# Optimization experiments

Hardware: AMD Instinct MI355X
Metric: run time of the kernel (lower is better)

The kernel has to match this reference:

```python
import jax, jax.numpy as jnp
import numpy as np


def setup_inputs() -> dict:
    key = jax.random.key(0)
    k1, k2 = jax.random.split(key)
    B, Q, K, H = 8, 2048, 2048, 128
    out_state = jax.random.normal(k1, (B, Q, H), dtype=jnp.float32)
    history = jax.random.normal(k2, (B, K, H), dtype=jnp.float32)
    return {"out_state": out_state, "history": history}


def reference(out_state, history):
    # tanh pre-activation on queries
    q = jnp.tanh(out_state)                              # [B, Q, H]
    # unscaled QK^T scores
    scores = jnp.einsum("bqh,bkh->bqk", q, history)      # [B, Q, K]
    probs = jax.nn.softmax(scores, axis=2)               # softmax over keys
    attn = jnp.einsum("bqk,bkh->bqh", probs, history)    # [B, Q, H]
    return attn
```

## Files before the change

kernel.cpp:

```cpp
#include <hip/hip_runtime.h>
#include <math.h>


typedef _Float16 half8 __attribute__((ext_vector_type(8)));
typedef _Float16 half4 __attribute__((ext_vector_type(4)));
typedef float    f32x4 __attribute__((ext_vector_type(4)));

#define QQ 2048
#define KK 2048
#define HH 128
#define BM 64
#define BN 64
#define NTILES 32
#define PS_STR 72
#define L2E 1.44269504f
#define SPLITS_TARGET 3

#define KS_STRP 136
#define VT_STRP 72

#define KH_HALVES     ((size_t)8 * KK * HH)
#define PREP_BYTES    (KH_HALVES * 4)
#define OSPLIT_BYTES  ((size_t)256 * BM * HH * 2)
#define MLSPLIT_FLOATS ((size_t)256 * BM)

union U32H { unsigned int u; _Float16 h[2]; };

typedef __attribute__((address_space(1))) const void gvoid;
typedef __attribute__((address_space(3))) void lvoid;

#define WAITVM4 asm volatile("s_waitcnt vmcnt(4)" ::: "memory")
#define WAITVM0 asm volatile("s_waitcnt vmcnt(0)" ::: "memory")
static __device__ __forceinline__ void wgbar() {
    asm volatile("" ::: "memory");
    __builtin_amdgcn_s_barrier();
    asm volatile("" ::: "memory");
}

__launch_bounds__(256)
__global__ void attn_prep(const float* __restrict__ history,
                          _Float16* __restrict__ wsh) {
    __shared__ __align__(16) _Float16 Ks[BN * KS_STRP];
    __shared__ __align__(16) _Float16 Vt[HH * VT_STRP];

    const int tid = threadIdx.x;
    const int bid = blockIdx.x;
    const int b   = bid >> 5;
    const int kt  = bid & 31;

    const float* hb = history + ((size_t)b * KK + (size_t)kt * BN) * HH;
    const int r0 = tid >> 5;
    const int c4 = (tid & 31) * 4;
    #pragma unroll
    for (int j = 0; j < 8; ++j) {
        const float4 g = *(const float4*)(hb + (size_t)(r0 + 8 * j) * HH + c4);
        half4 hv;
        hv[0] = (_Float16)g.x; hv[1] = (_Float16)g.y;
        hv[2] = (_Float16)g.z; hv[3] = (_Float16)g.w;
        *(half4*)&Ks[(r0 + 8 * j) * KS_STRP + c4] = hv;
    }
    __syncthreads();

    {
        const int h0  = 2 * (tid & 63);
        const int n0t = (tid >> 6) * 16;
        half8 ra0, ra1, rb0, rb1;
        #pragma unroll
        for (int i = 0; i < 8; ++i) {
            U32H t; t.u = *(const unsigned int*)&Ks[(n0t + i) * KS_STRP + h0];
            ra0[i] = t.h[0]; rb0[i] = t.h[1];
        }
        #pragma unroll
        for (int i = 8; i < 16; ++i) {
            U32H t; t.u = *(const unsigned int*)&Ks[(n0t + i) * KS_STRP + h0];
            ra1[i - 8] = t.h[0]; rb1[i - 8] = t.h[1];
        }
        *(half8*)&Vt[(h0    ) * VT_STRP + n0t    ] = ra0;
        *(half8*)&Vt[(h0    ) * VT_STRP + n0t + 8] = ra1;
        *(half8*)&Vt[(h0 + 1) * VT_STRP + n0t    ] = rb0;
        *(half8*)&Vt[(h0 + 1) * VT_STRP + n0t + 8] = rb1;
    }

    {
        const int k  = tid >> 2;
        const int c0 = (tid & 3) * 32;
        const int sk = (k & 7) << 3;
        _Float16* dst = wsh + ((size_t)b * KK + (size_t)kt * BN + k) * HH;
        #pragma unroll
        for (int g8 = 0; g8 < 4; ++g8)
            *(half8*)&dst[(c0 + 8 * g8) ^ sk] = *(const half8*)&Ks[k * KS_STRP + c0 + 8 * g8];
    }
    __syncthreads();

    {
        const int h  = tid >> 1;
        const int n0 = (tid & 1) * 32;
        const int th = (h & 7) << 3;
        _Float16* dst = wsh + KH_HALVES + (((size_t)b * NTILES + kt) * HH + h) * BN;
        #pragma unroll
        for (int g8 = 0; g8 < 4; ++g8)
            *(half8*)&dst[(n0 + 8 * g8) ^ th] = *(const half8*)&Vt[h * VT_STRP + n0 + 8 * g8];
    }
}

__launch_bounds__(256, 3)
__global__ void attn_main(const float* __restrict__ out_state,
                          const _Float16* __restrict__ wsh,
                          float* __restrict__ out,
                          char* __restrict__ wsb,
                          int splits) {
    __shared__ __align__(16) _Float16 Ks[BN * HH];
    __shared__ __align__(16) _Float16 Vt[HH * BN];
    __shared__ __align__(16) _Float16 Ps[4][16 * PS_STR];

    const int tid  = threadIdx.x;
    const int wave = tid >> 6;
    const int lane = tid & 63;
    const int quad = lane >> 4;
    const int lc   = lane & 15;
    const int swz  = (lc & 7) << 3;

    const int bid  = blockIdx.x;
    const int s    = bid >> 8;
    const int r256 = bid & 255;
    const int b    = r256 >> 5;
    const int qb   = r256 & 31;
    const int m0   = qb * BM;

    const int kt0 = (NTILES * s) / splits;
    const int kt1 = (NTILES * (s + 1)) / splits;

    const _Float16* khb = wsh + (size_t)b * KK * HH;
    const _Float16* vtb = wsh + KH_HALVES + (size_t)b * NTILES * (HH * BN);

    auto issueK = [&](int t) {
        const char* gsrc = (const char*)(khb + (size_t)t * (BN * HH));
        #pragma unroll
        for (int c = 0; c < 4; ++c) {
            const int off = (c * 4 + wave) * 1024 + lane * 16;
            __builtin_amdgcn_global_load_lds((gvoid*)(gsrc + off),
                                             (lvoid*)((char*)Ks + off), 16, 0, 0);
        }
    };
    auto issueV = [&](int t) {
        const char* gsrc = (const char*)(vtb + (size_t)t * (HH * BN));
        #pragma unroll
        for (int c = 0; c < 4; ++c) {
            const int off = (c * 4 + wave) * 1024 + lane * 16;
            __builtin_amdgcn_global_load_lds((gvoid*)(gsrc + off),
                                             (lvoid*)((char*)Vt + off), 16, 0, 0);
        }
    };

    issueK(kt0);
    issueV(kt0);

    half8 qf[4];
    {
        const int m = m0 + wave * 16 + lc;
        const float* qrow = out_state + ((size_t)b * QQ + m) * HH;
        float4 qa[8];
        #pragma unroll
        for (int s4 = 0; s4 < 4; ++s4) {
            qa[2 * s4]     = *(const float4*)(qrow + 32 * s4 + quad * 8);
            qa[2 * s4 + 1] = *(const float4*)(qrow + 32 * s4 + quad * 8 + 4);
        }
        #pragma unroll
        for (int s4 = 0; s4 < 4; ++s4) {
            qf[s4][0] = (_Float16)tanhf(qa[2*s4].x);   qf[s4][1] = (_Float16)tanhf(qa[2*s4].y);
            qf[s4][2] = (_Float16)tanhf(qa[2*s4].z);   qf[s4][3] = (_Float16)tanhf(qa[2*s4].w);
            qf[s4][4] = (_Float16)tanhf(qa[2*s4+1].x); qf[s4][5] = (_Float16)tanhf(qa[2*s4+1].y);
            qf[s4][6] = (_Float16)tanhf(qa[2*s4+1].z); qf[s4][7] = (_Float16)tanhf(qa[2*s4+1].w);
        }
    }

    const f32x4 zero4 = {0.f, 0.f, 0.f, 0.f};
    f32x4 O[8];
    #pragma unroll
    for (int i = 0; i < 8; ++i) O[i] = zero4;
    f32x4 Osum = zero4;
    float rmax = -3.0e38f;

    const half8 ones = {(_Float16)1.f,(_Float16)1.f,(_Float16)1.f,(_Float16)1.f,
                        (_Float16)1.f,(_Float16)1.f,(_Float16)1.f,(_Float16)1.f};

    for (int kt = kt0; kt < kt1; ++kt) {
        const bool more = (kt + 1 < kt1);

        WAITVM4;
        wgbar();

        f32x4 S[4];
        __builtin_amdgcn_s_setprio(1);
        #pragma unroll
        for (int nt = 0; nt < 4; ++nt) {
            f32x4 acc = zero4;
            #pragma unroll
            for (int s4 = 0; s4 < 4; ++s4) {
                const half8 kf = *(const half8*)
                    &Ks[((nt * 16 + lc) << 7) + ((32 * s4 + (quad << 3)) ^ swz)];
                acc = __builtin_amdgcn_mfma_f32_16x16x32_f16(kf, qf[s4], acc, 0, 0, 0);
            }
            S[nt] = acc;
        }
        __builtin_amdgcn_s_setprio(0);

        wgbar();
        if (more) issueK(kt + 1);

        float tmax = S[0][0];
        #pragma unroll
        for (int nt = 0; nt < 4; ++nt)
            #pragma unroll
            for (int r = 0; r < 4; ++r)
                tmax = fmaxf(tmax, S[nt][r]);
        tmax = fmaxf(tmax, __shfl_xor(tmax, 16, 64));
        tmax = fmaxf(tmax, __shfl_xor(tmax, 32, 64));

        if (!__all(tmax <= rmax)) {
            const float nm    = fmaxf(rmax, tmax);
            const float alpha = exp2f((rmax - nm) * L2E);
            rmax = nm;
            #pragma unroll
            for (int ct = 0; ct < 8; ++ct) O[ct] *= alpha;
            Osum *= alpha;
        }

        #pragma unroll
        for (int nt = 0; nt < 4; ++nt)
            #pragma unroll
            for (int r = 0; r < 4; ++r)
                S[nt][r] = exp2f((S[nt][r] - rmax) * L2E);

        #pragma unroll
        for (int nt = 0; nt < 4; ++nt) {
            half4 pv;
            pv[0] = (_Float16)S[nt][0]; pv[1] = (_Float16)S[nt][1];
            pv[2] = (_Float16)S[nt][2]; pv[3] = (_Float16)S[nt][3];
            *(half4*)&Ps[wave][lc * PS_STR + nt * 16 + quad * 4] = pv;
        }

        if (more) { WAITVM4; } else { WAITVM0; }
        wgbar();

        __builtin_amdgcn_s_setprio(1);
        #pragma unroll
        for (int s2 = 0; s2 < 2; ++s2) {
            const half8 pb = *(const half8*)&Ps[wave][lc * PS_STR + s2 * 32 + quad * 8];
            Osum = __builtin_amdgcn_mfma_f32_16x16x32_f16(ones, pb, Osum, 0, 0, 0);
            #pragma unroll
            for (int ct = 0; ct < 8; ++ct) {
                const half8 vf = *(const half8*)
                    &Vt[((ct * 16 + lc) << 6) + ((32 * s2 + (quad << 3)) ^ swz)];
                O[ct] = __builtin_amdgcn_mfma_f32_16x16x32_f16(vf, pb, O[ct], 0, 0, 0);
            }
        }
        __builtin_amdgcn_s_setprio(0);

        wgbar();
        if (more) issueV(kt + 1);
    }

    if (splits == 1) {
        const float inv = 1.0f / Osum[0];
        float* orow = out + ((size_t)b * QQ + m0 + wave * 16 + lc) * HH;
        #pragma unroll
        for (int ct = 0; ct < 8; ++ct) {
            f32x4 v = O[ct] * inv;
            *(f32x4*)&orow[ct * 16 + quad * 4] = v;
        }
    } else {
        const float inv = 1.0f / Osum[0];
        _Float16* oh = (_Float16*)(wsb + PREP_BYTES)
                     + ((size_t)(s * 256 + r256) * BM + wave * 16 + lc) * HH;
        #pragma unroll
        for (int ct = 0; ct < 8; ++ct) {
            const f32x4 v = O[ct] * inv;
            half4 hv;
            hv[0] = (_Float16)v[0]; hv[1] = (_Float16)v[1];
            hv[2] = (_Float16)v[2]; hv[3] = (_Float16)v[3];
            *(half4*)&oh[ct * 16 + quad * 4] = hv;
        }
        if (quad == 0) {
            float* wm = (float*)(wsb + PREP_BYTES + (size_t)splits * OSPLIT_BYTES);
            const size_t idx = (size_t)(s * 256 + r256) * BM + wave * 16 + lc;
            wm[idx] = rmax;
            wm[(size_t)splits * MLSPLIT_FLOATS + idx] = Osum[0];
        }
    }
}

__launch_bounds__(256)
__global__ void attn_combine(const char* __restrict__ wsb,
                             float* __restrict__ out,
                             int splits) {
    const int idx = blockIdx.x * 256 + threadIdx.x;
    const int h   = idx & 127;
    const int q   = (idx >> 7) & 2047;
    const int b   = idx >> 18;
    const int qb  = q >> 6;
    const int qr  = q & 63;
    const int blk = b * 32 + qb;

    const _Float16* oh = (const _Float16*)(wsb + PREP_BYTES);
    const float* wm = (const float*)(wsb + PREP_BYTES + (size_t)splits * OSPLIT_BYTES);
    const float* wl = wm + (size_t)splits * MLSPLIT_FLOATS;

    float ms[SPLITS_TARGET];
    float M = -3.0e38f;
    for (int s = 0; s < splits; ++s) {
        ms[s] = wm[(size_t)(s * 256 + blk) * BM + qr];
        M = fmaxf(M, ms[s]);
    }
    float denom = 0.f, val = 0.f;
    for (int s = 0; s < splits; ++s) {
        const float wgt = exp2f((ms[s] - M) * L2E) * wl[(size_t)(s * 256 + blk) * BM + qr];
        denom += wgt;
        val   += wgt * (float)oh[(size_t)(s * 256 + blk) * (BM * HH) + (size_t)qr * HH + h];
    }
    out[idx] = val / denom;
}

extern "C" void kernel_launch(void* const* d_in, const int* in_sizes, int n_in,
                              void* d_out, int out_size, void* d_ws, size_t ws_size,
                              hipStream_t stream) {
    const float* out_state = (const float*)d_in[0];
    const float* history   = (const float*)d_in[1];
    float* out = (float*)d_out;
    char* wsb  = (char*)d_ws;

    const size_t need3 = PREP_BYTES
                       + (size_t)SPLITS_TARGET * OSPLIT_BYTES
                       + (size_t)SPLITS_TARGET * 2 * MLSPLIT_FLOATS * 4;
    const int splits = (ws_size >= need3) ? SPLITS_TARGET : 1;

    attn_prep<<<dim3(256), dim3(256), 0, stream>>>(history, (_Float16*)wsb);
    attn_main<<<dim3(256 * splits), dim3(256), 0, stream>>>(out_state, (const _Float16*)wsb,
                                                            out, wsb, splits);
    if (splits > 1)
        attn_combine<<<dim3((8 * QQ * HH) / 256), dim3(256), 0, stream>>>(wsb, out, splits);
}
```

Measured before the change: 120.9 us.

## Fuse prep, main and combine into one cooperative kernel with grid syncs

Merges the three kernels (fp16 conversion/transpose of history, split attention, split combine) into one cooperative launch of 768 blocks that uses grid-wide syncs, removing two kernel launch gaps. The prep stage now writes swizzled tiles into LDS and copies them out linearly, and the combine handles two outputs per thread with vector stores. The cooperative path needs all 768 blocks resident at once (3 per CU on 256 CUs). It also adds the cost of grid barriers and falls back to separate launches if the cooperative launch fails.

```diff
diff --git a/kernel.cpp b/kernel.cpp
--- a/kernel.cpp
+++ b/kernel.cpp
@@ -1,10 +1,14 @@
 #include <hip/hip_runtime.h>
+#include <hip/hip_cooperative_groups.h>
 #include <math.h>
 
+
+namespace cg = cooperative_groups;
 
 typedef _Float16 half8 __attribute__((ext_vector_type(8)));
 typedef _Float16 half4 __attribute__((ext_vector_type(4)));
 typedef float    f32x4 __attribute__((ext_vector_type(4)));
+typedef float    f32x2 __attribute__((ext_vector_type(2)));
 
 #define QQ 2048
 #define KK 2048
@@ -14,15 +18,19 @@
 #define NTILES 32
 #define PS_STR 72
 #define L2E 1.44269504f
-#define SPLITS_TARGET 3
-
-#define KS_STRP 136
-#define VT_STRP 72
-
-#define KH_HALVES     ((size_t)8 * KK * HH)
-#define PREP_BYTES    (KH_HALVES * 4)
-#define OSPLIT_BYTES  ((size_t)256 * BM * HH * 2)
+#define SPLITS 3
+#define FUSED_BLOCKS (256 * SPLITS)
+
+#define KH_HALVES      ((size_t)8 * KK * HH)
+#define PREP_BYTES     (KH_HALVES * 4)
+#define OSPLIT_BYTES   ((size_t)256 * BM * HH * 2)
 #define MLSPLIT_FLOATS ((size_t)256 * BM)
+
+struct SharedMem {
+    _Float16 Ks[BN * HH];
+    _Float16 Vt[HH * BN];
+    _Float16 Ps[4][16 * PS_STR];
+};
 
 union U32H { unsigned int u; _Float16 h[2]; };
 
@@ -37,27 +45,23 @@
     asm volatile("" ::: "memory");
 }
 
-__launch_bounds__(256)
-__global__ void attn_prep(const float* __restrict__ history,
-                          _Float16* __restrict__ wsh) {
-    __shared__ __align__(16) _Float16 Ks[BN * KS_STRP];
-    __shared__ __align__(16) _Float16 Vt[HH * VT_STRP];
-
-    const int tid = threadIdx.x;
-    const int bid = blockIdx.x;
-    const int b   = bid >> 5;
-    const int kt  = bid & 31;
+static __device__ __forceinline__
+void do_prep(SharedMem* sm, const float* __restrict__ history,
+             _Float16* __restrict__ wsh, int bid, int tid) {
+    const int b  = bid >> 5;
+    const int kt = bid & 31;
 
     const float* hb = history + ((size_t)b * KK + (size_t)kt * BN) * HH;
     const int r0 = tid >> 5;
     const int c4 = (tid & 31) * 4;
     #pragma unroll
     for (int j = 0; j < 8; ++j) {
-        const float4 g = *(const float4*)(hb + (size_t)(r0 + 8 * j) * HH + c4);
+        const int k = r0 + 8 * j;
+        const float4 g = *(const float4*)(hb + (size_t)k * HH + c4);
         half4 hv;
         hv[0] = (_Float16)g.x; hv[1] = (_Float16)g.y;
         hv[2] = (_Float16)g.z; hv[3] = (_Float16)g.w;
-        *(half4*)&Ks[(r0 + 8 * j) * KS_STRP + c4] = hv;
+        *(half4*)&sm->Ks[k * HH + (c4 ^ ((k & 7) << 3))] = hv;
     }
     __syncthreads();
 
@@ -67,60 +71,46 @@
         half8 ra0, ra1, rb0, rb1;
         #pragma unroll
         for (int i = 0; i < 8; ++i) {
-            U32H t; t.u = *(const unsigned int*)&Ks[(n0t + i) * KS_STRP + h0];
+            const int n = n0t + i;
+            U32H t; t.u = *(const unsigned int*)&sm->Ks[n * HH + (h0 ^ ((n & 7) << 3))];
             ra0[i] = t.h[0]; rb0[i] = t.h[1];
         }
         #pragma unroll
         for (int i = 8; i < 16; ++i) {
-            U32H t; t.u = *(const unsigned int*)&Ks[(n0t + i) * KS_STRP + h0];
+            const int n = n0t + i;
+            U32H t; t.u = *(const unsigned int*)&sm->Ks[n * HH + (h0 ^ ((n & 7) << 3))];
             ra1[i - 8] = t.h[0]; rb1[i - 8] = t.h[1];
         }
-        *(half8*)&Vt[(h0    ) * VT_STRP + n0t    ] = ra0;
-        *(half8*)&Vt[(h0    ) * VT_STRP + n0t + 8] = ra1;
-        *(half8*)&Vt[(h0 + 1) * VT_STRP + n0t    ] = rb0;
-        *(half8*)&Vt[(h0 + 1) * VT_STRP + n0t + 8] = rb1;
-    }
-
-    {
-        const int k  = tid >> 2;
-        const int c0 = (tid & 3) * 32;
-        const int sk = (k & 7) << 3;
-        _Float16* dst = wsh + ((size_t)b * KK + (size_t)kt * BN + k) * HH;
-        #pragma unroll
-        for (int g8 = 0; g8 < 4; ++g8)
-            *(half8*)&dst[(c0 + 8 * g8) ^ sk] = *(const half8*)&Ks[k * KS_STRP + c0 + 8 * g8];
+        const int th0 = (h0 & 7) << 3;
+        const int th1 = ((h0 + 1) & 7) << 3;
+        *(half8*)&sm->Vt[(h0    ) * BN + ((n0t    ) ^ th0)] = ra0;
+        *(half8*)&sm->Vt[(h0    ) * BN + ((n0t + 8) ^ th0)] = ra1;
+        *(half8*)&sm->Vt[(h0 + 1) * BN + ((n0t    ) ^ th1)] = rb0;
+        *(half8*)&sm->Vt[(h0 + 1) * BN + ((n0t + 8) ^ th1)] = rb1;
     }
     __syncthreads();
 
-    {
-        const int h  = tid >> 1;
-        const int n0 = (tid & 1) * 32;
-        const int th = (h & 7) << 3;
-        _Float16* dst = wsh + KH_HALVES + (((size_t)b * NTILES + kt) * HH + h) * BN;
-        #pragma unroll
-        for (int g8 = 0; g8 < 4; ++g8)
-            *(half8*)&dst[(n0 + 8 * g8) ^ th] = *(const half8*)&Vt[h * VT_STRP + n0 + 8 * g8];
-    }
-}
-
-__launch_bounds__(256, 3)
-__global__ void attn_main(const float* __restrict__ out_state,
-                          const _Float16* __restrict__ wsh,
-                          float* __restrict__ out,
-                          char* __restrict__ wsb,
-                          int splits) {
-    __shared__ __align__(16) _Float16 Ks[BN * HH];
-    __shared__ __align__(16) _Float16 Vt[HH * BN];
-    __shared__ __align__(16) _Float16 Ps[4][16 * PS_STR];
-
-    const int tid  = threadIdx.x;
+    _Float16* kdst = wsh + ((size_t)b * KK + (size_t)kt * BN) * HH;
+    _Float16* vdst = wsh + KH_HALVES + ((size_t)(b * NTILES + kt)) * (HH * BN);
+    const f32x4* ksrc = (const f32x4*)sm->Ks;
+    const f32x4* vsrc = (const f32x4*)sm->Vt;
+    #pragma unroll
+    for (int i = 0; i < 4; ++i) {
+        ((f32x4*)kdst)[i * 256 + tid] = ksrc[i * 256 + tid];
+        ((f32x4*)vdst)[i * 256 + tid] = vsrc[i * 256 + tid];
+    }
+}
+
+static __device__ __forceinline__
+void do_main(SharedMem* sm, const float* __restrict__ out_state,
+             const _Float16* __restrict__ wsh, float* __restrict__ out,
+             char* __restrict__ wsb, int bid, int tid, int splits) {
     const int wave = tid >> 6;
     const int lane = tid & 63;
     const int quad = lane >> 4;
     const int lc   = lane & 15;
     const int swz  = (lc & 7) << 3;
 
-    const int bid  = blockIdx.x;
     const int s    = bid >> 8;
     const int r256 = bid & 255;
     const int b    = r256 >> 5;
@@ -139,7 +129,7 @@
         for (int c = 0; c < 4; ++c) {
             const int off = (c * 4 + wave) * 1024 + lane * 16;
             __builtin_amdgcn_global_load_lds((gvoid*)(gsrc + off),
-                                             (lvoid*)((char*)Ks + off), 16, 0, 0);
+                                             (lvoid*)((char*)sm->Ks + off), 16, 0, 0);
         }
     };
     auto issueV = [&](int t) {
@@ -148,7 +138,7 @@
         for (int c = 0; c < 4; ++c) {
             const int off = (c * 4 + wave) * 1024 + lane * 16;
             __builtin_amdgcn_global_load_lds((gvoid*)(gsrc + off),
-                                             (lvoid*)((char*)Vt + off), 16, 0, 0);
+                                             (lvoid*)((char*)sm->Vt + off), 16, 0, 0);
         }
     };
 
@@ -198,7 +188,7 @@
             #pragma unroll
             for (int s4 = 0; s4 < 4; ++s4) {
                 const half8 kf = *(const half8*)
-                    &Ks[((nt * 16 + lc) << 7) + ((32 * s4 + (quad << 3)) ^ swz)];
+                    &sm->Ks[((nt * 16 + lc) << 7) + ((32 * s4 + (quad << 3)) ^ swz)];
                 acc = __builtin_amdgcn_mfma_f32_16x16x32_f16(kf, qf[s4], acc, 0, 0, 0);
             }
             S[nt] = acc;
@@ -237,7 +227,7 @@
             half4 pv;
             pv[0] = (_Float16)S[nt][0]; pv[1] = (_Float16)S[nt][1];
             pv[2] = (_Float16)S[nt][2]; pv[3] = (_Float16)S[nt][3];
-            *(half4*)&Ps[wave][lc * PS_STR + nt * 16 + quad * 4] = pv;
+            *(half4*)&sm->Ps[wave][lc * PS_STR + nt * 16 + quad * 4] = pv;
         }
 
         if (more) { WAITVM4; } else { WAITVM0; }
@@ -246,12 +236,12 @@
         __builtin_amdgcn_s_setprio(1);
         #pragma unroll
         for (int s2 = 0; s2 < 2; ++s2) {
-            const half8 pb = *(const half8*)&Ps[wave][lc * PS_STR + s2 * 32 + quad * 8];
+            const half8 pb = *(const half8*)&sm->Ps[wave][lc * PS_STR + s2 * 32 + quad * 8];
             Osum = __builtin_amdgcn_mfma_f32_16x16x32_f16(ones, pb, Osum, 0, 0, 0);
             #pragma unroll
             for (int ct = 0; ct < 8; ++ct) {
                 const half8 vf = *(const half8*)
-                    &Vt[((ct * 16 + lc) << 6) + ((32 * s2 + (quad << 3)) ^ swz)];
+                    &sm->Vt[((ct * 16 + lc) << 6) + ((32 * s2 + (quad << 3)) ^ swz)];
                 O[ct] = __builtin_amdgcn_mfma_f32_16x16x32_f16(vf, pb, O[ct], 0, 0, 0);
             }
         }
@@ -290,14 +280,12 @@
     }
 }
 
-__launch_bounds__(256)
-__global__ void attn_combine(const char* __restrict__ wsb,
-                             float* __restrict__ out,
-                             int splits) {
-    const int idx = blockIdx.x * 256 + threadIdx.x;
-    const int h   = idx & 127;
-    const int q   = (idx >> 7) & 2047;
-    const int b   = idx >> 18;
+static __device__ __forceinline__
+void do_combine_pair(const char* __restrict__ wsb, float* __restrict__ out,
+                     int pid, int splits) {
+    const int h2  = pid & 63;
+    const int q   = (pid >> 6) & 2047;
+    const int b   = pid >> 17;
     const int qb  = q >> 6;
     const int qr  = q & 63;
     const int blk = b * 32 + qb;
@@ -306,19 +294,69 @@
     const float* wm = (const float*)(wsb + PREP_BYTES + (size_t)splits * OSPLIT_BYTES);
     const float* wl = wm + (size_t)splits * MLSPLIT_FLOATS;
 
-    float ms[SPLITS_TARGET];
+    float ms[SPLITS];
     float M = -3.0e38f;
     for (int s = 0; s < splits; ++s) {
         ms[s] = wm[(size_t)(s * 256 + blk) * BM + qr];
         M = fmaxf(M, ms[s]);
     }
-    float denom = 0.f, val = 0.f;
+    float denom = 0.f, v0 = 0.f, v1 = 0.f;
     for (int s = 0; s < splits; ++s) {
         const float wgt = exp2f((ms[s] - M) * L2E) * wl[(size_t)(s * 256 + blk) * BM + qr];
         denom += wgt;
-        val   += wgt * (float)oh[(size_t)(s * 256 + blk) * (BM * HH) + (size_t)qr * HH + h];
-    }
-    out[idx] = val / denom;
+        U32H t;
+        t.u = *(const unsigned int*)&oh[(size_t)(s * 256 + blk) * (BM * HH)
+                                        + (size_t)qr * HH + 2 * h2];
+        v0 += wgt * (float)t.h[0];
+        v1 += wgt * (float)t.h[1];
+    }
+    const float inv = 1.0f / denom;
+    f32x2 r; r[0] = v0 * inv; r[1] = v1 * inv;
+    *(f32x2*)&out[((size_t)(b * QQ + q)) * HH + 2 * h2] = r;
+}
+
+__launch_bounds__(256, 3)
+__global__ void attn_fused(const float* __restrict__ out_state,
+                           const float* __restrict__ history,
+                           float* __restrict__ out,
+                           char* __restrict__ wsb) {
+    __shared__ SharedMem sm;
+    const int tid = threadIdx.x;
+    const int bid = blockIdx.x;
+
+    if (bid < 256)
+        do_prep(&sm, history, (_Float16*)wsb, bid, tid);
+    cg::this_grid().sync();
+
+    do_main(&sm, out_state, (const _Float16*)wsb, out, wsb, bid, tid, SPLITS);
+    cg::this_grid().sync();
+
+    for (int pid = bid * 256 + tid; pid < (1 << 20); pid += FUSED_BLOCKS * 256)
+        do_combine_pair(wsb, out, pid, SPLITS);
+}
+
+__launch_bounds__(256)
+__global__ void attn_prep_k(const float* __restrict__ history,
+                            _Float16* __restrict__ wsh) {
+    __shared__ SharedMem sm;
+    do_prep(&sm, history, wsh, blockIdx.x, threadIdx.x);
+}
+
+__launch_bounds__(256, 3)
+__global__ void attn_main_k(const float* __restrict__ out_state,
+                            const _Float16* __restrict__ wsh,
+                            float* __restrict__ out,
+                            char* __restrict__ wsb,
+                            int splits) {
+    __shared__ SharedMem sm;
+    do_main(&sm, out_state, wsh, out, wsb, blockIdx.x, threadIdx.x, splits);
+}
+
+__launch_bounds__(256)
+__global__ void attn_combine_k(const char* __restrict__ wsb,
+                               float* __restrict__ out,
+                               int splits) {
+    do_combine_pair(wsb, out, blockIdx.x * 256 + threadIdx.x, splits);
 }
 
 extern "C" void kernel_launch(void* const* d_in, const int* in_sizes, int n_in,
@@ -330,13 +368,23 @@
     char* wsb  = (char*)d_ws;
 
     const size_t need3 = PREP_BYTES
-                       + (size_t)SPLITS_TARGET * OSPLIT_BYTES
-                       + (size_t)SPLITS_TARGET * 2 * MLSPLIT_FLOATS * 4;
-    const int splits = (ws_size >= need3) ? SPLITS_TARGET : 1;
-
-    attn_prep<<<dim3(256), dim3(256), 0, stream>>>(history, (_Float16*)wsb);
-    attn_main<<<dim3(256 * splits), dim3(256), 0, stream>>>(out_state, (const _Float16*)wsb,
-                                                            out, wsb, splits);
-    if (splits > 1)
-        attn_combine<<<dim3((8 * QQ * HH) / 256), dim3(256), 0, stream>>>(wsb, out, splits);
-}
+                       + (size_t)SPLITS * OSPLIT_BYTES
+                       + (size_t)SPLITS * 2 * MLSPLIT_FLOATS * 4;
+
+    if (ws_size >= need3) {
+        void* args[] = { (void*)&out_state, (void*)&history, (void*)&out, (void*)&wsb };
+        hipError_t e = hipLaunchCooperativeKernel((void*)attn_fused,
+                                                  dim3(FUSED_BLOCKS), dim3(256),
+                                                  args, 0, stream);
+        if (e == hipSuccess) return;
+        (void)hipGetLastError();
+        attn_prep_k<<<dim3(256), dim3(256), 0, stream>>>(history, (_Float16*)wsb);
+        attn_main_k<<<dim3(FUSED_BLOCKS), dim3(256), 0, stream>>>(out_state, (const _Float16*)wsb,
+                                                                  out, wsb, SPLITS);
+        attn_combine_k<<<dim3((1 << 20) / 256), dim3(256), 0, stream>>>(wsb, out, SPLITS);
+    } else {
+        attn_prep_k<<<dim3(256), dim3(256), 0, stream>>>(history, (_Float16*)wsb);
+        attn_main_k<<<dim3(256), dim3(256), 0, stream>>>(out_state, (const _Float16*)wsb,
+                                                         out, wsb, 1);
+    }
+}
```

Result: slower. 308.9 us (+155.5%).
